# Kernel optimization log

Hardware: AMD Instinct MI355X
Metric: run time of the kernel (lower is better)

## Reference

```python
import jax, jax.numpy as jnp
import numpy as np

EPS = 1e-5

def _batchnorm(x, gamma, beta):
    # training-mode BN: batch statistics over (N, T, V) per channel, biased var
    mean = jnp.mean(x, axis=(0, 2, 3), keepdims=True)
    var = jnp.var(x, axis=(0, 2, 3), keepdims=True)
    return (x - mean) * jax.lax.rsqrt(var + EPS) * gamma[None, :, None, None] + beta[None, :, None, None]

def _shift(x, s):
    # per-channel learnable temporal shift with linear interpolation, zero pad
    # x: (N, C, T, V), s: (C,) real-valued shift amounts
    N, C, T, V = x.shape
    t = jnp.arange(T, dtype=s.dtype)
    tsrc = t[None, :] + s[:, None]                      # (C, T) source positions
    i0 = jnp.floor(tsrc).astype(jnp.int32)
    frac = tsrc - i0.astype(s.dtype)
    i1 = i0 + 1
    w0 = (1.0 - frac) * ((i0 >= 0) & (i0 < T))          # zero outside bounds
    w1 = frac * ((i1 >= 0) & (i1 < T))
    i0c = jnp.clip(i0, 0, T - 1)
    i1c = jnp.clip(i1, 0, T - 1)
    cidx = jnp.arange(C)[:, None]                       # (C, 1) for gather
    x0 = x[:, cidx, i0c]                                # (N, C, T, V)
    x1 = x[:, cidx, i1c]
    return w0[None, :, :, None] * x0 + w1[None, :, :, None] * x1

def setup_inputs() -> dict:
    key = jax.random.key(0)
    ks = jax.random.split(key, 4)
    N, Cin, Cout, T, V = 64, 128, 256, 128, 25
    fan_out_scale = (2.0 / (Cout * 3 * 3)) ** 0.5       # kaiming_normal fan_out
    return {
        "x": jax.random.normal(ks[0], (N, Cin, T, V), jnp.float32),
        "bn1_gamma": jnp.ones((Cin,), jnp.float32),
        "bn1_beta": jnp.zeros((Cin,), jnp.float32),
        "shift_in_s": jax.random.normal(ks[1], (Cin,), jnp.float32) * 0.5,
        "conv_w": jax.random.normal(ks[2], (Cout, Cin, 3, 3), jnp.float32) * fan_out_scale,
        "conv_b": jnp.zeros((Cout,), jnp.float32),
        "shift_out_s": jax.random.normal(ks[3], (Cout,), jnp.float32) * 0.5,
        "bn2_gamma": jnp.ones((Cout,), jnp.float32),
        "bn2_beta": jnp.zeros((Cout,), jnp.float32),
    }

def reference(x, bn1_gamma, bn1_beta, shift_in_s, conv_w, conv_b, shift_out_s, bn2_gamma, bn2_beta):
    h = _batchnorm(x, bn1_gamma, bn1_beta)
    h = _shift(h, shift_in_s)
    h = jax.lax.conv_general_dilated(
        h, conv_w, window_strides=(2, 2), padding=((1, 1), (1, 1)),
        dimension_numbers=("NCHW", "OIHW", "NCHW"))
    h = h + conv_b[None, :, None, None]
    h = jax.nn.relu(h)
    h = _shift(h, shift_out_s)
    return _batchnorm(h, bn2_gamma, bn2_beta)
```

## Files before the change

### kernel.cpp

```cpp
#include <hip/hip_runtime.h>
#include <hip/hip_bf16.h>

#define N_    64
#define CIN   128
#define COUT  256
#define T_    128
#define V_    25
#define TOUT  64
#define VOUT  13
#define EPS_  1e-5f

typedef __hip_bfloat16 bf16;
typedef __attribute__((ext_vector_type(8))) short short8x;
typedef __attribute__((ext_vector_type(4))) float f32x4;

__device__ __forceinline__ float ldv(const bf16* p)  { return __bfloat162float(*p); }
__device__ __forceinline__ float ldv(const float* p) { return *p; }
__device__ __forceinline__ void  stv(bf16* p, float v)  { *p = __float2bfloat16(v); }
__device__ __forceinline__ void  stv(float* p, float v) { *p = v; }

__device__ __forceinline__ unsigned bf16rne(float f) {
    unsigned u = __float_as_uint(f);
    return (u + 0x7FFFu + ((u >> 16) & 1u)) >> 16;
}

__device__ __forceinline__ float ldnt(const float* p) { return __builtin_nontemporal_load(p); }
__device__ __forceinline__ float ldnt(const bf16* p) {
    unsigned short u = __builtin_nontemporal_load((const unsigned short*)p);
    return __uint_as_float((unsigned)u << 16);
}
__device__ __forceinline__ void stnt(float* p, float v) { __builtin_nontemporal_store(v, p); }
__device__ __forceinline__ void stnt(bf16* p, float v) {
    unsigned short u = (unsigned short)bf16rne(v);
    __builtin_nontemporal_store(u, (unsigned short*)p);
}

__device__ __forceinline__ void load4(const float* p, float& a, float& b, float& c, float& d) {
    float4 v = *reinterpret_cast<const float4*>(p);
    a = v.x; b = v.y; c = v.z; d = v.w;
}
__device__ __forceinline__ void load4(const bf16* p, float& a, float& b, float& c, float& d) {
    ushort4 u = *reinterpret_cast<const ushort4*>(p);
    a = __uint_as_float((unsigned)u.x << 16);
    b = __uint_as_float((unsigned)u.y << 16);
    c = __uint_as_float((unsigned)u.z << 16);
    d = __uint_as_float((unsigned)u.w << 16);
}

__device__ __forceinline__ void blockReduce2(float& s, float& ss) {
    __shared__ float ls[4], lss[4];
    int lane = threadIdx.x & 63, wid = threadIdx.x >> 6;
#pragma unroll
    for (int o = 32; o > 0; o >>= 1) {
        s  += __shfl_down(s, o, 64);
        ss += __shfl_down(ss, o, 64);
    }
    if (lane == 0) { ls[wid] = s; lss[wid] = ss; }
    __syncthreads();
    if (threadIdx.x == 0) {
        s  = ls[0] + ls[1] + ls[2] + ls[3];
        ss = lss[0] + lss[1] + lss[2] + lss[3];
    }
}

__global__ void detect_k(const unsigned short* __restrict__ xr, int* flag,
                         float* __restrict__ s1, float* __restrict__ q1,
                         float* __restrict__ s2, float* __restrict__ q2) {
    if (threadIdx.x < CIN) { s1[threadIdx.x] = 0.f; q1[threadIdx.x] = 0.f; }
    s2[threadIdx.x] = 0.f; q2[threadIdx.x] = 0.f;
    __shared__ int cnt;
    if (threadIdx.x == 0) cnt = 0;
    __syncthreads();
    int c = 0;
    for (int i = threadIdx.x; i < 8192; i += 256) {
        int e = (xr[i] >> 7) & 0xFF;
        if (e >= 192) c++;
    }
    atomicAdd(&cnt, c);
    __syncthreads();
    if (threadIdx.x == 0) flag[0] = (cnt > 0) ? 1 : 0;
}

template<int MODE, typename DT>
__global__ __launch_bounds__(256) void wprep_k(const int* __restrict__ flag,
                                               const DT* __restrict__ wgt,
                                               unsigned* __restrict__ wfrag) {
    if (flag[0] != MODE) return;
    const int total = 2304 * 256;
    for (int o = blockIdx.x * 256 + threadIdx.x; o < total; o += gridDim.x * 256) {
        int j    = o & 3;
        int lane = (o >> 2) & 63;
        int f    = o >> 8;
        int ch   = f & 7;
        int ctg  = (f >> 3) & 15;
        int pp   = f >> 7;
        int pass = pp & 1;
        int tap  = pp >> 1;
        int co = ctg * 16 + (lane & 15);
        int ci = ch * 16 + (lane >> 4) * 4 + j;
        float w = ldv(&wgt[((size_t)co * CIN + ci) * 9 + tap]);
        unsigned hb = bf16rne(w);
        unsigned val;
        if (pass == 0) {
            val = hb | (hb << 16);
        } else {
            float hif = __uint_as_float(hb << 16);
            unsigned lb = bf16rne(w - hif);
            val = lb | (lb << 16);
        }
        wfrag[o] = val;
    }
}

template<int MODE, typename DT>
__global__ __launch_bounds__(256) void bn1_k(const int* __restrict__ flag,
                                             const DT* __restrict__ x,
                                             float* __restrict__ s1, float* __restrict__ q1) {
    if (flag[0] != MODE) return;
    const int c  = blockIdx.x;
    const int n0 = blockIdx.y * (N_ / 4);
    float s = 0.f, ss = 0.f;
    for (int idx = threadIdx.x; idx < (N_ / 4) * 800; idx += 256) {
        int n = n0 + idx / 800;
        int q = idx - (idx / 800) * 800;
        const DT* xp = x + ((size_t)n * CIN + c) * (T_ * V_) + q * 4;
        float v0, v1, v2, v3;
        load4(xp, v0, v1, v2, v3);
        s  += (v0 + v1) + (v2 + v3);
        ss += (v0 * v0 + v1 * v1) + (v2 * v2 + v3 * v3);
    }
    blockReduce2(s, ss);
    if (threadIdx.x == 0) { atomicAdd(&s1[c], s); atomicAdd(&q1[c], ss); }
}

template<int MODE, typename DT>
__global__ void bn1fin_k(const int* __restrict__ flag,
                         const DT* __restrict__ gamma, const DT* __restrict__ beta,
                         const float* __restrict__ s1, const float* __restrict__ q1,
                         float* __restrict__ a1, float* __restrict__ b1) {
    if (flag[0] != MODE) return;
    int c = threadIdx.x;
    float cnt = (float)(N_ * T_ * V_);
    float mean = s1[c] / cnt;
    float var = q1[c] / cnt - mean * mean;
    float a = ldv(&gamma[c]) * rsqrtf(var + EPS_);
    a1[c] = a;
    b1[c] = ldv(&beta[c]) - mean * a;
}

#define CHUNK 16
#define CIPAD 20
template<int MODE, typename DT>
__global__ __launch_bounds__(256, 4) void conv_mfma_k(const int* __restrict__ flag,
                                                      const DT* __restrict__ x,
                                                      const unsigned* __restrict__ wfrag,
                                                      const DT* __restrict__ bias,
                                                      const DT* __restrict__ s_in,
                                                      const float* __restrict__ a1,
                                                      const float* __restrict__ b1,
                                                      DT* __restrict__ y) {
    if (flag[0] != MODE) return;
    __shared__ __align__(16) unsigned shp[9 * 27 * CIPAD];
    const int tg    = blockIdx.x;
    const int n     = blockIdx.y;
    const int tid   = threadIdx.x;
    const int wv    = tid >> 6;
    const int lane  = tid & 63;
    const int khi   = lane >> 4;
    const int ln16  = lane & 15;
    const int tbase = 8 * tg - 1;

    const short8x* wfl = reinterpret_cast<const short8x*>(wfrag) + lane;
    const short8x* shv = reinterpret_cast<const short8x*>(shp);

    f32x4 acc[4][4];
#pragma unroll
    for (int ct = 0; ct < 4; ct++)
#pragma unroll
        for (int tt = 0; tt < 4; tt++) acc[ct][tt] = (f32x4){0.f, 0.f, 0.f, 0.f};

#pragma unroll 1
    for (int ch = 0; ch < 8; ch++) {
        __syncthreads();
#pragma unroll 4
        for (int it = 0; it < 16; it++) {
            int e = it * 256 + tid;
            if (e < CHUNK * 9 * 27) {
                int vv = e % 27;
                int r0 = e / 27;
                int lt = r0 % 9;
                int ci = r0 / 9;
                int gci  = ch * 16 + ci;
                int t_in = tbase + lt;
                int v_in = vv - 1;
                float hv = 0.f;
                if (t_in >= 0 && t_in < T_ && v_in >= 0 && v_in < V_) {
                    float s = ldv(&s_in[gci]);
                    float tsrc = (float)t_in + s;
                    float f0 = floorf(tsrc);
                    float frac = tsrc - f0;
                    int i0 = (int)f0;
                    int i1 = i0 + 1;
                    float w0 = (i0 >= 0 && i0 < T_) ? (1.f - frac) : 0.f;
                    float w1 = (i1 >= 0 && i1 < T_) ? frac : 0.f;
                    int i0c = min(max(i0, 0), T_ - 1);
                    int i1c = min(max(i1, 0), T_ - 1);
                    const DT* xc = x + ((size_t)n * CIN + gci) * (T_ * V_);
                    float xv = w0 * ldnt(&xc[i0c * V_ + v_in]) + w1 * ldnt(&xc[i1c * V_ + v_in]);
                    hv = a1[gci] * xv + b1[gci] * (w0 + w1);
                }
                unsigned hb = bf16rne(hv);
                float hif = __uint_as_float(hb << 16);
                unsigned lb = bf16rne(hv - hif);
                shp[(lt * 27 + vv) * CIPAD + ci] = hb | (lb << 16);
            }
        }
        __syncthreads();

#pragma unroll 1
        for (int kt = 0; kt < 3; kt++) {
#pragma unroll
            for (int kv = 0; kv < 3; kv++) {
                const int tap = kt * 3 + kv;
                const int vvc = min(2 * ln16 + kv, 26);
                short8x af[2][4];
#pragma unroll
                for (int pass = 0; pass < 2; pass++)
#pragma unroll
                    for (int ct = 0; ct < 4; ct++)
                        af[pass][ct] = wfl[(size_t)((((tap * 2 + pass) * 16 + wv * 4 + ct) * 8 + ch)) * 64];
#pragma unroll
                for (int tt = 0; tt < 4; tt++) {
                    const int lt = 2 * tt + kt;
                    short8x b = shv[(lt * 27 + vvc) * (CIPAD / 4) + khi];
#pragma unroll
                    for (int pass = 0; pass < 2; pass++)
#pragma unroll
                        for (int ct = 0; ct < 4; ct++)
                            acc[ct][tt] = __builtin_amdgcn_mfma_f32_16x16x32_bf16(af[pass][ct], b, acc[ct][tt], 0, 0, 0);
                }
            }
        }
    }

    if (ln16 < VOUT) {
#pragma unroll
        for (int ct = 0; ct < 4; ct++) {
#pragma unroll
            for (int r = 0; r < 4; r++) {
                const int co = wv * 64 + ct * 16 + khi * 4 + r;
                const float bi = ldv(&bias[co]);
#pragma unroll
                for (int tt = 0; tt < 4; tt++) {
                    const int to = tg * 4 + tt;
                    DT* yp = y + (((size_t)n * COUT + co) * TOUT + to) * VOUT;
                    stnt(&yp[ln16], fmaxf(acc[ct][tt][r] + bi, 0.f));
                }
            }
        }
    }
}

template<int MODE, typename DT>
__global__ __launch_bounds__(256) void bn2_k(const int* __restrict__ flag, const DT* __restrict__ y,
                                             const DT* __restrict__ s_out,
                                             float* __restrict__ s2, float* __restrict__ q2) {
    if (flag[0] != MODE) return;
    int co = blockIdx.x;
    int n0 = blockIdx.y * (N_ / 4);
    float sv = ldv(&s_out[co]);
    float s = 0.f, ss = 0.f;
    for (int i = threadIdx.x; i < (N_ / 4) * TOUT * VOUT; i += 256) {
        int n = n0 + i / (TOUT * VOUT);
        int r = i % (TOUT * VOUT);
        int to = r / VOUT;
        int vo = r % VOUT;
        float tsrc = (float)to + sv;
        float f0 = floorf(tsrc);
        float frac = tsrc - f0;
        int i0 = (int)f0, i1 = i0 + 1;
        float w0 = (i0 >= 0 && i0 < TOUT) ? (1.f - frac) : 0.f;
        float w1 = (i1 >= 0 && i1 < TOUT) ? frac : 0.f;
        int i0c = min(max(i0, 0), TOUT - 1);
        int i1c = min(max(i1, 0), TOUT - 1);
        const DT* yc = y + ((size_t)n * COUT + co) * (TOUT * VOUT);
        float z = w0 * ldv(&yc[i0c * VOUT + vo]) + w1 * ldv(&yc[i1c * VOUT + vo]);
        s += z; ss += z * z;
    }
    blockReduce2(s, ss);
    if (threadIdx.x == 0) { atomicAdd(&s2[co], s); atomicAdd(&q2[co], ss); }
}

template<int MODE, typename DT>
__global__ void bn2fin_k(const int* __restrict__ flag,
                         const DT* __restrict__ gamma, const DT* __restrict__ beta,
                         const float* __restrict__ s2, const float* __restrict__ q2,
                         float* __restrict__ a2, float* __restrict__ b2) {
    if (flag[0] != MODE) return;
    int c = threadIdx.x;
    float cnt = (float)(N_ * TOUT * VOUT);
    float mean = s2[c] / cnt;
    float var = q2[c] / cnt - mean * mean;
    float a = ldv(&gamma[c]) * rsqrtf(var + EPS_);
    a2[c] = a;
    b2[c] = ldv(&beta[c]) - mean * a;
}

template<int MODE, typename DT>
__global__ void final_k(const int* __restrict__ flag, DT* __restrict__ y,
                        const DT* __restrict__ s_out,
                        const float* __restrict__ a2, const float* __restrict__ b2) {
    if (flag[0] != MODE) return;
    __shared__ float pl[TOUT * VOUT];
    int co = blockIdx.x, n = blockIdx.y;
    DT* base = y + ((size_t)n * COUT + co) * (TOUT * VOUT);
    for (int i = threadIdx.x; i < TOUT * VOUT; i += 256) pl[i] = ldv(&base[i]);
    __syncthreads();
    float sv = ldv(&s_out[co]);
    float A = a2[co], B = b2[co];
    for (int i = threadIdx.x; i < TOUT * VOUT; i += 256) {
        int to = i / VOUT, vo = i % VOUT;
        float tsrc = (float)to + sv;
        float f0 = floorf(tsrc);
        float frac = tsrc - f0;
        int i0 = (int)f0, i1 = i0 + 1;
        float w0 = (i0 >= 0 && i0 < TOUT) ? (1.f - frac) : 0.f;
        float w1 = (i1 >= 0 && i1 < TOUT) ? frac : 0.f;
        int i0c = min(max(i0, 0), TOUT - 1);
        int i1c = min(max(i1, 0), TOUT - 1);
        float z = w0 * pl[i0c * VOUT + vo] + w1 * pl[i1c * VOUT + vo];
        stv(&base[i], A * z + B);
    }
}

extern "C" void kernel_launch(void* const* d_in, const int* in_sizes, int n_in,
                              void* d_out, int out_size, void* d_ws, size_t ws_size,
                              hipStream_t stream) {
    int*   flag = (int*)d_ws;
    float* a1 = (float*)((char*)d_ws + 256);
    float* b1 = a1 + 128;
    float* a2 = b1 + 128;
    float* b2 = a2 + 256;
    float* s1 = b2 + 256;
    float* q1 = s1 + 128;
    float* s2 = q1 + 128;
    float* q2 = s2 + 256;
    unsigned* wfrag = (unsigned*)((char*)d_ws + 8192);

    detect_k<<<1, 256, 0, stream>>>((const unsigned short*)d_in[0], flag, s1, q1, s2, q2);

    const bf16* xb    = (const bf16*)d_in[0];
    const bf16* g1b   = (const bf16*)d_in[1];
    const bf16* be1b  = (const bf16*)d_in[2];
    const bf16* sinb  = (const bf16*)d_in[3];
    const bf16* wbb   = (const bf16*)d_in[4];
    const bf16* cbb   = (const bf16*)d_in[5];
    const bf16* soutb = (const bf16*)d_in[6];
    const bf16* g2b   = (const bf16*)d_in[7];
    const bf16* be2b  = (const bf16*)d_in[8];
    bf16* yb = (bf16*)d_out;
    const float* xf    = (const float*)d_in[0];
    const float* g1f   = (const float*)d_in[1];
    const float* be1f  = (const float*)d_in[2];
    const float* sinf_ = (const float*)d_in[3];
    const float* wbf   = (const float*)d_in[4];
    const float* cbf   = (const float*)d_in[5];
    const float* soutf = (const float*)d_in[6];
    const float* g2f   = (const float*)d_in[7];
    const float* be2f  = (const float*)d_in[8];
    float* yf = (float*)d_out;

    wprep_k<0, bf16> <<<dim3(576), 256, 0, stream>>>(flag, wbb, wfrag);
    wprep_k<1, float><<<dim3(576), 256, 0, stream>>>(flag, wbf, wfrag);

    bn1_k<0, bf16> <<<dim3(CIN, 4), 256, 0, stream>>>(flag, xb, s1, q1);
    bn1_k<1, float><<<dim3(CIN, 4), 256, 0, stream>>>(flag, xf, s1, q1);
    bn1fin_k<0, bf16> <<<1, 128, 0, stream>>>(flag, g1b, be1b, s1, q1, a1, b1);
    bn1fin_k<1, float><<<1, 128, 0, stream>>>(flag, g1f, be1f, s1, q1, a1, b1);

    conv_mfma_k<0, bf16> <<<dim3(TOUT / 4, N_), 256, 0, stream>>>(flag, xb, wfrag, cbb, sinb, a1, b1, yb);
    conv_mfma_k<1, float><<<dim3(TOUT / 4, N_), 256, 0, stream>>>(flag, xf, wfrag, cbf, sinf_, a1, b1, yf);

    bn2_k<0, bf16> <<<dim3(COUT, 4), 256, 0, stream>>>(flag, yb, soutb, s2, q2);
    bn2_k<1, float><<<dim3(COUT, 4), 256, 0, stream>>>(flag, yf, soutf, s2, q2);
    bn2fin_k<0, bf16> <<<1, 256, 0, stream>>>(flag, g2b, be2b, s2, q2, a2, b2);
    bn2fin_k<1, float><<<1, 256, 0, stream>>>(flag, g2f, be2f, s2, q2, a2, b2);

    final_k<0, bf16> <<<dim3(COUT, N_), 256, 0, stream>>>(flag, yb, soutb, a2, b2);
    final_k<1, float><<<dim3(COUT, N_), 256, 0, stream>>>(flag, yf, soutf, a2, b2);
}
```

Baseline: 528.1 us.

## Merge dtype-dispatched kernels, fold BN finalize into consumers, drop lo*lo MFMA pass

Each pair of per-dtype kernels becomes a single kernel that branches on the flag at runtime, and the BN1/BN2 finalize kernels are folded into the conv and final kernels. Together this cuts the launch count from about 13 to 6. The conv kernel now stages hi and lo bf16 planes separately with 32-channel chunks and issues three MFMAs (hi*hi, hi*lo, lo*hi) instead of four, skipping the lo*lo product. The weight prep is also re-laid out and the smem fill loop is reorganised so shift parameters are hoisted per channel. The costs are a larger shared-memory footprint, which may reduce occupancy, and slightly lower precision from the dropped lo*lo term.

```diff
diff --git a/kernel.cpp b/kernel.cpp
--- a/kernel.cpp
+++ b/kernel.cpp
@@ -9,6 +9,8 @@
 #define TOUT  64
 #define VOUT  13
 #define EPS_  1e-5f
+#define CNT1  ((float)(N_ * T_ * V_))
+#define CNT2  ((float)(N_ * TOUT * VOUT))
 
 typedef __hip_bfloat16 bf16;
 typedef __attribute__((ext_vector_type(8))) short short8x;
@@ -81,42 +83,37 @@
     if (threadIdx.x == 0) flag[0] = (cnt > 0) ? 1 : 0;
 }
 
-template<int MODE, typename DT>
-__global__ __launch_bounds__(256) void wprep_k(const int* __restrict__ flag,
-                                               const DT* __restrict__ wgt,
-                                               unsigned* __restrict__ wfrag) {
-    if (flag[0] != MODE) return;
-    const int total = 2304 * 256;
-    for (int o = blockIdx.x * 256 + threadIdx.x; o < total; o += gridDim.x * 256) {
-        int j    = o & 3;
-        int lane = (o >> 2) & 63;
-        int f    = o >> 8;
-        int ch   = f & 7;
-        int ctg  = (f >> 3) & 15;
-        int pp   = f >> 7;
-        int pass = pp & 1;
-        int tap  = pp >> 1;
-        int co = ctg * 16 + (lane & 15);
-        int ci = ch * 16 + (lane >> 4) * 4 + j;
-        float w = ldv(&wgt[((size_t)co * CIN + ci) * 9 + tap]);
+template<typename DT>
+__device__ __forceinline__ void prep_body(const DT* __restrict__ wgt, unsigned short* __restrict__ wf) {
+    int gid  = blockIdx.x * 256 + threadIdx.x;
+    int lane = gid & 63;
+    int f    = gid >> 6;
+    int ch   = f & 3;
+    int ctg  = (f >> 2) & 15;
+    int kind = (f >> 6) & 1;
+    int tap  = f >> 7;
+    int co   = ctg * 16 + (lane & 15);
+    int cib  = ch * 32 + (lane >> 4) * 8;
+    unsigned short o[8];
+#pragma unroll
+    for (int j = 0; j < 8; j++) {
+        float w = ldv(&wgt[((size_t)co * CIN + cib + j) * 9 + tap]);
         unsigned hb = bf16rne(w);
-        unsigned val;
-        if (pass == 0) {
-            val = hb | (hb << 16);
-        } else {
-            float hif = __uint_as_float(hb << 16);
-            unsigned lb = bf16rne(w - hif);
-            val = lb | (lb << 16);
-        }
-        wfrag[o] = val;
-    }
-}
-
-template<int MODE, typename DT>
-__global__ __launch_bounds__(256) void bn1_k(const int* __restrict__ flag,
-                                             const DT* __restrict__ x,
-                                             float* __restrict__ s1, float* __restrict__ q1) {
-    if (flag[0] != MODE) return;
+        if (kind == 0) o[j] = (unsigned short)hb;
+        else           o[j] = (unsigned short)bf16rne(w - __uint_as_float(hb << 16));
+    }
+    *reinterpret_cast<ushort4*>(wf + (size_t)gid * 8)     = make_ushort4(o[0], o[1], o[2], o[3]);
+    *reinterpret_cast<ushort4*>(wf + (size_t)gid * 8 + 4) = make_ushort4(o[4], o[5], o[6], o[7]);
+}
+__global__ __launch_bounds__(256) void prep_k(const int* __restrict__ flag,
+                                              const void* __restrict__ w, unsigned short* __restrict__ wf) {
+    if (flag[0]) prep_body<float>((const float*)w, wf);
+    else         prep_body<bf16>((const bf16*)w, wf);
+}
+
+template<typename DT>
+__device__ __forceinline__ void bn1_body(const DT* __restrict__ x,
+                                         float* __restrict__ s1, float* __restrict__ q1) {
     const int c  = blockIdx.x;
     const int n0 = blockIdx.y * (N_ / 4);
     float s = 0.f, ss = 0.f;
@@ -132,46 +129,40 @@
     blockReduce2(s, ss);
     if (threadIdx.x == 0) { atomicAdd(&s1[c], s); atomicAdd(&q1[c], ss); }
 }
-
-template<int MODE, typename DT>
-__global__ void bn1fin_k(const int* __restrict__ flag,
-                         const DT* __restrict__ gamma, const DT* __restrict__ beta,
-                         const float* __restrict__ s1, const float* __restrict__ q1,
-                         float* __restrict__ a1, float* __restrict__ b1) {
-    if (flag[0] != MODE) return;
-    int c = threadIdx.x;
-    float cnt = (float)(N_ * T_ * V_);
-    float mean = s1[c] / cnt;
-    float var = q1[c] / cnt - mean * mean;
-    float a = ldv(&gamma[c]) * rsqrtf(var + EPS_);
-    a1[c] = a;
-    b1[c] = ldv(&beta[c]) - mean * a;
-}
-
-#define CHUNK 16
-#define CIPAD 20
-template<int MODE, typename DT>
-__global__ __launch_bounds__(256, 4) void conv_mfma_k(const int* __restrict__ flag,
-                                                      const DT* __restrict__ x,
-                                                      const unsigned* __restrict__ wfrag,
-                                                      const DT* __restrict__ bias,
-                                                      const DT* __restrict__ s_in,
-                                                      const float* __restrict__ a1,
-                                                      const float* __restrict__ b1,
-                                                      DT* __restrict__ y) {
-    if (flag[0] != MODE) return;
-    __shared__ __align__(16) unsigned shp[9 * 27 * CIPAD];
-    const int tg    = blockIdx.x;
-    const int n     = blockIdx.y;
-    const int tid   = threadIdx.x;
-    const int wv    = tid >> 6;
-    const int lane  = tid & 63;
-    const int khi   = lane >> 4;
-    const int ln16  = lane & 15;
+__global__ __launch_bounds__(256) void bn1_k(const int* __restrict__ flag, const void* __restrict__ x,
+                                             float* __restrict__ s1, float* __restrict__ q1) {
+    if (flag[0]) bn1_body<float>((const float*)x, s1, q1);
+    else         bn1_body<bf16>((const bf16*)x, s1, q1);
+}
+
+#define HPLANE (9 * 27 * 40)
+template<typename DT>
+__device__ __forceinline__ void conv_body(const DT* __restrict__ x, const unsigned short* __restrict__ wf,
+                                          const DT* __restrict__ bias, const DT* __restrict__ s_in,
+                                          const DT* __restrict__ g1, const DT* __restrict__ be1,
+                                          const float* __restrict__ s1, const float* __restrict__ q1,
+                                          DT* __restrict__ y,
+                                          short* hp, float* a1s, float* b1s) {
+    const int tg   = blockIdx.x;
+    const int n    = blockIdx.y;
+    const int tid  = threadIdx.x;
+    const int wv   = tid >> 6;
+    const int lane = tid & 63;
+    const int khi  = lane >> 4;
+    const int ln16 = lane & 15;
     const int tbase = 8 * tg - 1;
 
-    const short8x* wfl = reinterpret_cast<const short8x*>(wfrag) + lane;
-    const short8x* shv = reinterpret_cast<const short8x*>(shp);
+    if (tid < CIN) {
+        float mean = s1[tid] / CNT1;
+        float var  = q1[tid] / CNT1 - mean * mean;
+        float a = ldv(&g1[tid]) * rsqrtf(var + EPS_);
+        a1s[tid] = a;
+        b1s[tid] = ldv(&be1[tid]) - mean * a;
+    }
+    __syncthreads();
+
+    const short8x* wfv = reinterpret_cast<const short8x*>(wf);
+    const short8x* shv = reinterpret_cast<const short8x*>(hp);
 
     f32x4 acc[4][4];
 #pragma unroll
@@ -179,40 +170,44 @@
 #pragma unroll
         for (int tt = 0; tt < 4; tt++) acc[ct][tt] = (f32x4){0.f, 0.f, 0.f, 0.f};
 
+    const int vvt  = tid & 31;
+    const int ci8  = tid >> 5;
+    const int v_in = vvt - 1;
+    const bool vok = (vvt >= 1) && (vvt <= 25);
+
 #pragma unroll 1
-    for (int ch = 0; ch < 8; ch++) {
+    for (int ch = 0; ch < 4; ch++) {
         __syncthreads();
-#pragma unroll 4
-        for (int it = 0; it < 16; it++) {
-            int e = it * 256 + tid;
-            if (e < CHUNK * 9 * 27) {
-                int vv = e % 27;
-                int r0 = e / 27;
-                int lt = r0 % 9;
-                int ci = r0 / 9;
-                int gci  = ch * 16 + ci;
-                int t_in = tbase + lt;
-                int v_in = vv - 1;
-                float hv = 0.f;
-                if (t_in >= 0 && t_in < T_ && v_in >= 0 && v_in < V_) {
-                    float s = ldv(&s_in[gci]);
-                    float tsrc = (float)t_in + s;
-                    float f0 = floorf(tsrc);
-                    float frac = tsrc - f0;
-                    int i0 = (int)f0;
-                    int i1 = i0 + 1;
-                    float w0 = (i0 >= 0 && i0 < T_) ? (1.f - frac) : 0.f;
-                    float w1 = (i1 >= 0 && i1 < T_) ? frac : 0.f;
-                    int i0c = min(max(i0, 0), T_ - 1);
-                    int i1c = min(max(i1, 0), T_ - 1);
-                    const DT* xc = x + ((size_t)n * CIN + gci) * (T_ * V_);
-                    float xv = w0 * ldnt(&xc[i0c * V_ + v_in]) + w1 * ldnt(&xc[i1c * V_ + v_in]);
-                    hv = a1[gci] * xv + b1[gci] * (w0 + w1);
+        if (vvt < 27) {
+#pragma unroll 1
+            for (int cq = 0; cq < 4; cq++) {
+                const int ci_l = cq * 8 + ci8;
+                const int gci  = ch * 32 + ci_l;
+                const float sv  = ldv(&s_in[gci]);
+                const float a1v = a1s[gci], b1v = b1s[gci];
+                const float fs = floorf(sv);
+                const float fr = sv - fs;
+                const int  ifs = (int)fs;
+                const DT* xc = x + ((size_t)n * CIN + gci) * (T_ * V_);
+#pragma unroll
+                for (int lt = 0; lt < 9; lt++) {
+                    const int t_in = tbase + lt;
+                    const int i0 = t_in + ifs, i1 = i0 + 1;
+                    float w0 = (i0 >= 0 && i0 < T_) ? (1.f - fr) : 0.f;
+                    float w1 = (i1 >= 0 && i1 < T_) ? fr : 0.f;
+                    float hv = 0.f;
+                    if (vok && t_in >= 0 && t_in < T_) {
+                        int i0c = min(max(i0, 0), T_ - 1);
+                        int i1c = min(max(i1, 0), T_ - 1);
+                        float xv = w0 * ldnt(&xc[i0c * V_ + v_in]) + w1 * ldnt(&xc[i1c * V_ + v_in]);
+                        hv = a1v * xv + b1v * (w0 + w1);
+                    }
+                    unsigned hb = bf16rne(hv);
+                    unsigned lb = bf16rne(hv - __uint_as_float(hb << 16));
+                    int rb = (lt * 27 + vvt) * 40 + ci_l;
+                    hp[rb]          = (short)hb;
+                    hp[HPLANE + rb] = (short)lb;
                 }
-                unsigned hb = bf16rne(hv);
-                float hif = __uint_as_float(hb << 16);
-                unsigned lb = bf16rne(hv - hif);
-                shp[(lt * 27 + vv) * CIPAD + ci] = hb | (lb << 16);
             }
         }
         __syncthreads();
@@ -223,21 +218,28 @@
             for (int kv = 0; kv < 3; kv++) {
                 const int tap = kt * 3 + kv;
                 const int vvc = min(2 * ln16 + kv, 26);
-                short8x af[2][4];
-#pragma unroll
-                for (int pass = 0; pass < 2; pass++)
-#pragma unroll
-                    for (int ct = 0; ct < 4; ct++)
-                        af[pass][ct] = wfl[(size_t)((((tap * 2 + pass) * 16 + wv * 4 + ct) * 8 + ch)) * 64];
+                short8x ahi[4], alo[4];
+#pragma unroll
+                for (int ct = 0; ct < 4; ct++) {
+                    const int fh = tap * 128 + (wv * 4 + ct) * 4 + ch;
+                    ahi[ct] = wfv[(size_t)fh * 64 + lane];
+                    alo[ct] = wfv[(size_t)(fh + 64) * 64 + lane];
+                }
 #pragma unroll
                 for (int tt = 0; tt < 4; tt++) {
                     const int lt = 2 * tt + kt;
-                    short8x b = shv[(lt * 27 + vvc) * (CIPAD / 4) + khi];
-#pragma unroll
-                    for (int pass = 0; pass < 2; pass++)
-#pragma unroll
-                        for (int ct = 0; ct < 4; ct++)
-                            acc[ct][tt] = __builtin_amdgcn_mfma_f32_16x16x32_bf16(af[pass][ct], b, acc[ct][tt], 0, 0, 0);
+                    const int rbase = (lt * 27 + vvc) * 5;
+                    short8x bh = shv[rbase + khi];
+                    short8x bl = shv[9 * 27 * 5 + rbase + khi];
+#pragma unroll
+                    for (int ct = 0; ct < 4; ct++)
+                        acc[ct][tt] = __builtin_amdgcn_mfma_f32_16x16x32_bf16(ahi[ct], bh, acc[ct][tt], 0, 0, 0);
+#pragma unroll
+                    for (int ct = 0; ct < 4; ct++)
+                        acc[ct][tt] = __builtin_amdgcn_mfma_f32_16x16x32_bf16(ahi[ct], bl, acc[ct][tt], 0, 0, 0);
+#pragma unroll
+                    for (int ct = 0; ct < 4; ct++)
+                        acc[ct][tt] = __builtin_amdgcn_mfma_f32_16x16x32_bf16(alo[ct], bh, acc[ct][tt], 0, 0, 0);
                 }
             }
         }
@@ -261,11 +263,25 @@
     }
 }
 
-template<int MODE, typename DT>
-__global__ __launch_bounds__(256) void bn2_k(const int* __restrict__ flag, const DT* __restrict__ y,
-                                             const DT* __restrict__ s_out,
-                                             float* __restrict__ s2, float* __restrict__ q2) {
-    if (flag[0] != MODE) return;
+__global__ __launch_bounds__(256, 4) void conv_k(const int* __restrict__ flag,
+                                                 const void* __restrict__ x, const unsigned short* __restrict__ wf,
+                                                 const void* __restrict__ bias, const void* __restrict__ s_in,
+                                                 const void* __restrict__ g1, const void* __restrict__ be1,
+                                                 const float* __restrict__ s1, const float* __restrict__ q1,
+                                                 void* __restrict__ y) {
+    __shared__ __align__(16) short hp[2 * HPLANE];
+    __shared__ float a1s[CIN], b1s[CIN];
+    if (flag[0])
+        conv_body<float>((const float*)x, wf, (const float*)bias, (const float*)s_in,
+                         (const float*)g1, (const float*)be1, s1, q1, (float*)y, hp, a1s, b1s);
+    else
+        conv_body<bf16>((const bf16*)x, wf, (const bf16*)bias, (const bf16*)s_in,
+                        (const bf16*)g1, (const bf16*)be1, s1, q1, (bf16*)y, hp, a1s, b1s);
+}
+
+template<typename DT>
+__device__ __forceinline__ void bn2_body(const DT* __restrict__ y, const DT* __restrict__ s_out,
+                                         float* __restrict__ s2, float* __restrict__ q2) {
     int co = blockIdx.x;
     int n0 = blockIdx.y * (N_ / 4);
     float sv = ldv(&s_out[co]);
@@ -290,34 +306,31 @@
     blockReduce2(s, ss);
     if (threadIdx.x == 0) { atomicAdd(&s2[co], s); atomicAdd(&q2[co], ss); }
 }
-
-template<int MODE, typename DT>
-__global__ void bn2fin_k(const int* __restrict__ flag,
-                         const DT* __restrict__ gamma, const DT* __restrict__ beta,
-                         const float* __restrict__ s2, const float* __restrict__ q2,
-                         float* __restrict__ a2, float* __restrict__ b2) {
-    if (flag[0] != MODE) return;
-    int c = threadIdx.x;
-    float cnt = (float)(N_ * TOUT * VOUT);
-    float mean = s2[c] / cnt;
-    float var = q2[c] / cnt - mean * mean;
-    float a = ldv(&gamma[c]) * rsqrtf(var + EPS_);
-    a2[c] = a;
-    b2[c] = ldv(&beta[c]) - mean * a;
-}
-
-template<int MODE, typename DT>
-__global__ void final_k(const int* __restrict__ flag, DT* __restrict__ y,
-                        const DT* __restrict__ s_out,
-                        const float* __restrict__ a2, const float* __restrict__ b2) {
-    if (flag[0] != MODE) return;
-    __shared__ float pl[TOUT * VOUT];
+__global__ __launch_bounds__(256) void bn2_k(const int* __restrict__ flag, const void* __restrict__ y,
+                                             const void* __restrict__ s_out,
+                                             float* __restrict__ s2, float* __restrict__ q2) {
+    if (flag[0]) bn2_body<float>((const float*)y, (const float*)s_out, s2, q2);
+    else         bn2_body<bf16>((const bf16*)y, (const bf16*)s_out, s2, q2);
+}
+
+template<typename DT>
+__device__ __forceinline__ void final_body(DT* __restrict__ y, const DT* __restrict__ s_out,
+                                           const DT* __restrict__ g2, const DT* __restrict__ be2,
+                                           const float* __restrict__ s2, const float* __restrict__ q2,
+                                           float* pl, float* ab) {
     int co = blockIdx.x, n = blockIdx.y;
     DT* base = y + ((size_t)n * COUT + co) * (TOUT * VOUT);
+    if (threadIdx.x == 0) {
+        float mean = s2[co] / CNT2;
+        float var  = q2[co] / CNT2 - mean * mean;
+        float a = ldv(&g2[co]) * rsqrtf(var + EPS_);
+        ab[0] = a;
+        ab[1] = ldv(&be2[co]) - mean * a;
+    }
     for (int i = threadIdx.x; i < TOUT * VOUT; i += 256) pl[i] = ldv(&base[i]);
     __syncthreads();
     float sv = ldv(&s_out[co]);
-    float A = a2[co], B = b2[co];
+    float A = ab[0], B = ab[1];
     for (int i = threadIdx.x; i < TOUT * VOUT; i += 256) {
         int to = i / VOUT, vo = i % VOUT;
         float tsrc = (float)to + sv;
@@ -332,60 +345,31 @@
         stv(&base[i], A * z + B);
     }
 }
+__global__ __launch_bounds__(256) void final_k(const int* __restrict__ flag, void* __restrict__ y,
+                                               const void* __restrict__ s_out,
+                                               const void* __restrict__ g2, const void* __restrict__ be2,
+                                               const float* __restrict__ s2, const float* __restrict__ q2) {
+    __shared__ float pl[TOUT * VOUT];
+    __shared__ float ab[2];
+    if (flag[0]) final_body<float>((float*)y, (const float*)s_out, (const float*)g2, (const float*)be2, s2, q2, pl, ab);
+    else         final_body<bf16>((bf16*)y, (const bf16*)s_out, (const bf16*)g2, (const bf16*)be2, s2, q2, pl, ab);
+}
 
 extern "C" void kernel_launch(void* const* d_in, const int* in_sizes, int n_in,
                               void* d_out, int out_size, void* d_ws, size_t ws_size,
                               hipStream_t stream) {
     int*   flag = (int*)d_ws;
-    float* a1 = (float*)((char*)d_ws + 256);
-    float* b1 = a1 + 128;
-    float* a2 = b1 + 128;
-    float* b2 = a2 + 256;
-    float* s1 = b2 + 256;
+    float* s1 = (float*)((char*)d_ws + 256);
     float* q1 = s1 + 128;
     float* s2 = q1 + 128;
     float* q2 = s2 + 256;
-    unsigned* wfrag = (unsigned*)((char*)d_ws + 8192);
+    unsigned short* wf = (unsigned short*)((char*)d_ws + 8192);
 
     detect_k<<<1, 256, 0, stream>>>((const unsigned short*)d_in[0], flag, s1, q1, s2, q2);
-
-    const bf16* xb    = (const bf16*)d_in[0];
-    const bf16* g1b   = (const bf16*)d_in[1];
-    const bf16* be1b  = (const bf16*)d_in[2];
-    const bf16* sinb  = (const bf16*)d_in[3];
-    const bf16* wbb   = (const bf16*)d_in[4];
-    const bf16* cbb   = (const bf16*)d_in[5];
-    const bf16* soutb = (const bf16*)d_in[6];
-    const bf16* g2b   = (const bf16*)d_in[7];
-    const bf16* be2b  = (const bf16*)d_in[8];
-    bf16* yb = (bf16*)d_out;
-    const float* xf    = (const float*)d_in[0];
-    const float* g1f   = (const float*)d_in[1];
-    const float* be1f  = (const float*)d_in[2];
-    const float* sinf_ = (const float*)d_in[3];
-    const float* wbf   = (const float*)d_in[4];
-    const float* cbf   = (const float*)d_in[5];
-    const float* soutf = (const float*)d_in[6];
-    const float* g2f   = (const float*)d_in[7];
-    const float* be2f  = (const float*)d_in[8];
-    float* yf = (float*)d_out;
-
-    wprep_k<0, bf16> <<<dim3(576), 256, 0, stream>>>(flag, wbb, wfrag);
-    wprep_k<1, float><<<dim3(576), 256, 0, stream>>>(flag, wbf, wfrag);
-
-    bn1_k<0, bf16> <<<dim3(CIN, 4), 256, 0, stream>>>(flag, xb, s1, q1);
-    bn1_k<1, float><<<dim3(CIN, 4), 256, 0, stream>>>(flag, xf, s1, q1);
-    bn1fin_k<0, bf16> <<<1, 128, 0, stream>>>(flag, g1b, be1b, s1, q1, a1, b1);
-    bn1fin_k<1, float><<<1, 128, 0, stream>>>(flag, g1f, be1f, s1, q1, a1, b1);
-
-    conv_mfma_k<0, bf16> <<<dim3(TOUT / 4, N_), 256, 0, stream>>>(flag, xb, wfrag, cbb, sinb, a1, b1, yb);
-    conv_mfma_k<1, float><<<dim3(TOUT / 4, N_), 256, 0, stream>>>(flag, xf, wfrag, cbf, sinf_, a1, b1, yf);
-
-    bn2_k<0, bf16> <<<dim3(COUT, 4), 256, 0, stream>>>(flag, yb, soutb, s2, q2);
-    bn2_k<1, float><<<dim3(COUT, 4), 256, 0, stream>>>(flag, yf, soutf, s2, q2);
-    bn2fin_k<0, bf16> <<<1, 256, 0, stream>>>(flag, g2b, be2b, s2, q2, a2, b2);
-    bn2fin_k<1, float><<<1, 256, 0, stream>>>(flag, g2f, be2f, s2, q2, a2, b2);
-
-    final_k<0, bf16> <<<dim3(COUT, N_), 256, 0, stream>>>(flag, yb, soutb, a2, b2);
-    final_k<1, float><<<dim3(COUT, N_), 256, 0, stream>>>(flag, yf, soutf, a2, b2);
-}
+    prep_k  <<<dim3(288), 256, 0, stream>>>(flag, d_in[4], wf);
+    bn1_k   <<<dim3(CIN, 4), 256, 0, stream>>>(flag, d_in[0], s1, q1);
+    conv_k  <<<dim3(TOUT / 4, N_), 256, 0, stream>>>(flag, d_in[0], wf, d_in[5], d_in[3],
+                                                     d_in[1], d_in[2], s1, q1, d_out);
+    bn2_k   <<<dim3(COUT, 4), 256, 0, stream>>>(flag, d_out, d_in[6], s2, q2);
+    final_k <<<dim3(COUT, N_), 256, 0, stream>>>(flag, d_out, d_in[6], d_in[7], d_in[8], s2, q2);
+}
```

After: 484.6 us. 8.2% less time.
